# Kernel tuning notes

Hardware: AMD Instinct MI355X
Metric: run time of the kernel (lower is better)

Reference implementation:

```python
import jax, jax.numpy as jnp
import numpy as np
import math

B, S, D, H, L, V, MAXLEN = 4, 2047, 256, 8, 2, 32000, 2048
DK = D // H
DFF = 2 * D
EPS = 1e-5


def make_pe(max_len, d):
    pos = jnp.arange(max_len, dtype=jnp.float32)[:, None]
    div = jnp.exp(jnp.arange(0, d, 2, dtype=jnp.float32) * (-math.log(10000.0) / d))
    pe = jnp.zeros((max_len, d), dtype=jnp.float32)
    pe = pe.at[:, 0::2].set(jnp.sin(pos * div))
    pe = pe.at[:, 1::2].set(jnp.cos(pos * div))
    return pe[None]  # [1, max_len, d]


def setup_inputs() -> dict:
    key = jax.random.key(0)
    ks = jax.random.split(key, 16)
    s = 0.02
    T = S + 1
    return {
        "embeddings": jax.random.normal(ks[0], (B, D), jnp.float32),
        "output_tokens": jax.random.randint(ks[1], (B, S), 0, V, jnp.int64),
        "causal_mask": jnp.tril(jnp.ones((T, T), jnp.int32))[None, None],  # [1,1,T,T]
        "key_padding_mask": jnp.ones((B, 1, 1, T), jnp.int32),
        "tok_emb": jax.random.normal(ks[2], (V, D), jnp.float32) * s,
        "pe": make_pe(MAXLEN, D),
        "Wq": jax.random.normal(ks[3], (L, D, D), jnp.float32) * s,
        "Wk": jax.random.normal(ks[4], (L, D, D), jnp.float32) * s,
        "Wv": jax.random.normal(ks[5], (L, D, D), jnp.float32) * s,
        "Wo": jax.random.normal(ks[6], (L, D, D), jnp.float32) * s,
        "bo": jnp.zeros((L, D), jnp.float32),
        "ln1_g": jnp.ones((L, D), jnp.float32),
        "ln1_b": jnp.zeros((L, D), jnp.float32),
        "W1": jax.random.normal(ks[7], (L, D, DFF), jnp.float32) * s,
        "b1": jnp.zeros((L, DFF), jnp.float32),
        "W2": jax.random.normal(ks[8], (L, DFF, D), jnp.float32) * s,
        "b2": jnp.zeros((L, D), jnp.float32),
        "ln2_g": jnp.ones((L, D), jnp.float32),
        "ln2_b": jnp.zeros((L, D), jnp.float32),
    }


def layer_norm(x, g, b):
    mu = jnp.mean(x, axis=-1, keepdims=True)
    var = jnp.mean(jnp.square(x - mu), axis=-1, keepdims=True)
    return (x - mu) * jax.lax.rsqrt(var + EPS) * g + b


def attention(x, Wq, Wk, Wv, Wo, bo, causal_mask, key_padding_mask):
    b, t, d = x.shape
    q = (x @ Wq).reshape(b, t, H, DK)
    k = (x @ Wk).reshape(b, t, H, DK)
    v = (x @ Wv).reshape(b, t, H, DK)
    scores = jnp.einsum('bqhd,bkhd->bhqk', q, k) / math.sqrt(DK)  # [B,H,T,T]
    neg = jnp.float32(-jnp.inf)
    scores = jnp.where(causal_mask == 0, neg, scores)
    scores = jnp.where(key_padding_mask == 0, neg, scores)
    attn = jax.nn.softmax(scores, axis=-1)
    out = jnp.einsum('bhqk,bkhd->bqhd', attn, v).reshape(b, t, d)
    return out @ Wo + bo


def reference(embeddings, output_tokens, causal_mask, key_padding_mask,
              tok_emb, pe, Wq, Wk, Wv, Wo, bo, ln1_g, ln1_b,
              W1, b1, W2, b2, ln2_g, ln2_b):
    emb_tok = tok_emb[output_tokens]                       # [B,S,D]
    x = jnp.concatenate([embeddings[:, None, :], emb_tok], axis=1)  # [B,T,D]
    x = x + pe[:, :x.shape[1]]
    for l in range(L):
        a = attention(x, Wq[l], Wk[l], Wv[l], Wo[l], bo[l], causal_mask, key_padding_mask)
        x = layer_norm(x + a, ln1_g[l], ln1_b[l])
        ff = jax.nn.relu(x @ W1[l] + b1[l]) @ W2[l] + b2[l]
        x = layer_norm(x + ff, ln2_g[l], ln2_b[l])
    return x[:, 1:, :]  # drop the prepended embedding position
```

## Files before the change

kernel.cpp:

```cpp
#include <hip/hip_runtime.h>
#include <cstdint>
#include <cstddef>

#define B_   4
#define S_   2047
#define T_   2048
#define D_   256
#define H_   8
#define DK_  32
#define DFF_ 512
#define L_   2

typedef short          s8v  __attribute__((ext_vector_type(8)));
typedef float          f4v  __attribute__((ext_vector_type(4)));
typedef unsigned short u4v  __attribute__((ext_vector_type(4)));
typedef unsigned short u8v  __attribute__((ext_vector_type(8)));
typedef unsigned int   u2v  __attribute__((ext_vector_type(2)));
typedef unsigned int   uint32;

union U8 { u8v v; unsigned short e[8]; };

__device__ __forceinline__ float bf2f(unsigned short h) {
    unsigned int u = ((unsigned int)h) << 16;
    float f; __builtin_memcpy(&f, &u, 4); return f;
}
__device__ __forceinline__ unsigned short f2bf(float f) {
    unsigned int u; __builtin_memcpy(&u, &f, 4);
    u += 0x7fffu + ((u >> 16) & 1u);
    return (unsigned short)(u >> 16);
}
__device__ __forceinline__ uint32 pack_bf2(float lo, float hi) {
    uint32 a, b;
    __builtin_memcpy(&a, &lo, 4); __builtin_memcpy(&b, &hi, 4);
    a += 0x8000u; b += 0x8000u;
    return __builtin_amdgcn_perm(b, a, 0x07060302);
}

#define QSCALE2 0.25503485951542068f

__global__ __launch_bounds__(256) void prep_k(
    const float* __restrict__ emb, const int* __restrict__ toks,
    const float* __restrict__ tokE, const float* __restrict__ pe,
    unsigned short* __restrict__ X,
    const float* __restrict__ Wq, const float* __restrict__ Wk,
    const float* __restrict__ Wv, const float* __restrict__ Wo,
    const float* __restrict__ W1, const float* __restrict__ W2,
    unsigned short* __restrict__ WqkvT, unsigned short* __restrict__ WoT,
    unsigned short* __restrict__ W1T, unsigned short* __restrict__ W2T)
{
    __shared__ float tile[32][33];
    if (blockIdx.x < 1024) {
        int idx = blockIdx.x * 256 + threadIdx.x;
        int d8 = (idx & 31) * 8;
        int t  = (idx >> 5) & (T_ - 1);
        int b  = idx >> 16;
        const float* src = (t == 0) ? (emb + b * D_)
                                    : (tokE + (size_t)toks[b * S_ + t - 1] * D_);
        const float* p = pe + (size_t)t * D_ + d8;
        U8 o;
#pragma unroll
        for (int j = 0; j < 8; ++j) o.e[j] = f2bf(src[d8 + j] + p[j]);
        *(u8v*)(X + (size_t)(b * T_ + t) * D_ + d8) = o.v;
        return;
    }
    int idx = blockIdx.x - 1024;
    const float* src; unsigned short* dst; int R, C, tr, tc;
    if (idx < 512) {
        int w = idx >> 7, rem = idx & 127, l = rem >> 6, t = rem & 63;
        tr = t >> 3; tc = t & 7; R = 256; C = 256;
        src = (w == 0 ? Wq : w == 1 ? Wk : w == 2 ? Wv : Wo) + (size_t)l * 65536;
        dst = (w < 3) ? WqkvT + (size_t)l * 196608 + (size_t)w * 65536
                      : WoT + (size_t)l * 65536;
    } else if (idx < 768) {
        int rem = idx - 512, l = rem >> 7, t = rem & 127;
        tr = t >> 4; tc = t & 15; R = 256; C = 512;
        src = W1 + (size_t)l * 131072; dst = W1T + (size_t)l * 131072;
    } else {
        int rem = idx - 768, l = rem >> 7, t = rem & 127;
        tr = t >> 3; tc = t & 7; R = 512; C = 256;
        src = W2 + (size_t)l * 131072; dst = W2T + (size_t)l * 131072;
    }
    int x = threadIdx.x & 31, y = threadIdx.x >> 5;
    int r0 = tr * 32, c0 = tc * 32;
#pragma unroll
    for (int i = 0; i < 32; i += 8) tile[y + i][x] = src[(size_t)(r0 + y + i) * C + c0 + x];
    __syncthreads();
#pragma unroll
    for (int i = 0; i < 32; i += 8)
        dst[(size_t)(c0 + y + i) * R + r0 + x] = f2bf(tile[x][y + i]);
}

__global__ __launch_bounds__(256) void gemm64_k(
    const unsigned short* __restrict__ A, const unsigned short* __restrict__ WT,
    const float* __restrict__ bias,
    unsigned short* __restrict__ oq, unsigned short* __restrict__ ok,
    unsigned short* __restrict__ ov, unsigned short* __restrict__ out,
    int K, int Ntot, int mode)
{
    __shared__ unsigned short At[64 * 72];
    __shared__ unsigned short Wt[64 * 72];
    const int tid = threadIdx.x;
    const int wave = tid >> 6, lane = tid & 63, l15 = lane & 15, quad = lane >> 4;
    const int m0 = blockIdx.x * 64, n0g = blockIdx.y * 64;

    f4v acc[4];
#pragma unroll
    for (int i = 0; i < 4; ++i) acc[i] = (f4v){0.f, 0.f, 0.f, 0.f};

    const int arow = tid >> 2, acg = (tid & 3) * 16;
    const unsigned short* ag = A + (size_t)(m0 + arow) * K + acg;
    const unsigned short* wg = WT + (size_t)(n0g + arow) * K + acg;
    u8v a0 = *(const u8v*)ag, a1 = *(const u8v*)(ag + 8);
    u8v w0 = *(const u8v*)wg, w1 = *(const u8v*)(wg + 8);

    const int niter = K >> 6;
    for (int kk = 0; kk < niter; ++kk) {
        *(u8v*)&At[arow * 72 + acg] = a0; *(u8v*)&At[arow * 72 + acg + 8] = a1;
        *(u8v*)&Wt[arow * 72 + acg] = w0; *(u8v*)&Wt[arow * 72 + acg + 8] = w1;
        __syncthreads();
        if (kk + 1 < niter) {
            int o = (kk + 1) * 64;
            a0 = *(const u8v*)(ag + o); a1 = *(const u8v*)(ag + o + 8);
            w0 = *(const u8v*)(wg + o); w1 = *(const u8v*)(wg + o + 8);
        }
#pragma unroll
        for (int ks = 0; ks < 2; ++ks) {
            s8v aF = *(const s8v*)&At[(wave * 16 + l15) * 72 + ks * 32 + quad * 8];
#pragma unroll
            for (int nt = 0; nt < 4; ++nt) {
                s8v wF = *(const s8v*)&Wt[(nt * 16 + l15) * 72 + ks * 32 + quad * 8];
                acc[nt] = __builtin_amdgcn_mfma_f32_16x16x32_bf16(aF, wF, acc[nt], 0, 0, 0);
            }
        }
        __syncthreads();
    }

    const int b = m0 >> 11, t0 = m0 & (T_ - 1);
    if (mode == 0) {
        int sub = blockIdx.y >> 2;
        int cb  = (blockIdx.y & 3) * 64;
        if (sub < 2) {
            unsigned short* dst = sub ? ok : oq;
            float sc = sub ? 1.f : QSCALE2;
#pragma unroll
            for (int nt = 0; nt < 4; ++nt) {
                int c = cb + nt * 16 + l15, hh = c >> 5, dk = c & 31;
#pragma unroll
                for (int r = 0; r < 4; ++r) {
                    int t = t0 + wave * 16 + quad * 4 + r;
                    dst[((size_t)(b * H_ + hh) * T_ + t) * DK_ + dk] = f2bf(acc[nt][r] * sc);
                }
            }
        } else {
            unsigned short* Vb = At;
#pragma unroll
            for (int nt = 0; nt < 4; ++nt) {
                int base = (nt * 16 + l15) * 72 + wave * 16 + quad * 4;
                *(uint32*)&Vb[base]     = pack_bf2(acc[nt][0], acc[nt][1]);
                *(uint32*)&Vb[base + 2] = pack_bf2(acc[nt][2], acc[nt][3]);
            }
            __syncthreads();
            int c = tid >> 2, chunk = tid & 3;
            int cg = cb + c, hh = cg >> 5, dk = cg & 31;
            unsigned short* dst = ov + ((size_t)(b * H_ + hh) * DK_ + dk) * T_ + t0 + chunk * 16;
            u8v v0 = *(u8v*)&Vb[c * 72 + chunk * 16];
            u8v v1 = *(u8v*)&Vb[c * 72 + chunk * 16 + 8];
            *(u8v*)dst = v0; *(u8v*)(dst + 8) = v1;
        }
    } else {
#pragma unroll
        for (int nt = 0; nt < 4; ++nt) {
            int c = n0g + nt * 16 + l15;
            float bv = bias[c];
#pragma unroll
            for (int r = 0; r < 4; ++r) {
                float v = acc[nt][r] + bv;
                v = v > 0.f ? v : 0.f;
                out[(size_t)(m0 + wave * 16 + quad * 4 + r) * Ntot + c] = f2bf(v);
            }
        }
    }
}

__global__ __launch_bounds__(512) void tail32_k(
    const unsigned short* __restrict__ AO,
    const unsigned short* __restrict__ WoTl, const float* __restrict__ bo,
    const unsigned short* __restrict__ Xres,
    const float* __restrict__ g1, const float* __restrict__ be1,
    const unsigned short* __restrict__ W1Tl, const float* __restrict__ b1,
    const unsigned short* __restrict__ W2Tl, const float* __restrict__ b2,
    const float* __restrict__ g2, const float* __restrict__ be2,
    unsigned short* __restrict__ Xout, float* __restrict__ fout, int last)
{
    __shared__ unsigned short Wt[256 * 72];
    __shared__ unsigned short As[32 * 72];
    __shared__ unsigned short X1s[32 * 264];
    __shared__ unsigned short Hs[32 * 520];
    __shared__ float LNsc[256];

    const int tid = threadIdx.x;
    const int wave = tid >> 6, lane = tid & 63, l15 = lane & 15, quad = lane >> 4;
    const int wr = wave >> 2, wc = wave & 3;
    const int m0 = blockIdx.x * 32;
    const int rbase = wr * 16 + quad * 4;

    const int wrow = tid >> 1, wcol = (tid & 1) * 32;
    const int arow = tid >> 3, acol = (tid & 7) * 8;

    f4v acc[4];
    u8v w0, w1, w2, w3, a0 = {0,0,0,0,0,0,0,0};

    const unsigned short* wgo = WoTl + (size_t)wrow * 256 + wcol;
    const unsigned short* wg1 = W1Tl + (size_t)wrow * 256 + wcol;
    const unsigned short* wg1b = W1Tl + (size_t)(256 + wrow) * 256 + wcol;
    const unsigned short* wg2 = W2Tl + (size_t)wrow * 512 + wcol;
    const unsigned short* ag  = AO + (size_t)(m0 + arow) * 256 + acol;

#define LDW(p, o) { w0 = *(const u8v*)((p)+(o)); w1 = *(const u8v*)((p)+(o)+8); \
                    w2 = *(const u8v*)((p)+(o)+16); w3 = *(const u8v*)((p)+(o)+24); }
#define STW { *(u8v*)&Wt[wrow*72+wcol] = w0; *(u8v*)&Wt[wrow*72+wcol+8] = w1; \
              *(u8v*)&Wt[wrow*72+wcol+16] = w2; *(u8v*)&Wt[wrow*72+wcol+24] = w3; }

#pragma unroll
    for (int i = 0; i < 4; ++i) acc[i] = (f4v){0.f, 0.f, 0.f, 0.f};
    LDW(wgo, 0);
    if (tid < 256) a0 = *(const u8v*)ag;
    for (int kk = 0; kk < 4; ++kk) {
        STW;
        if (tid < 256) *(u8v*)&As[arow * 72 + acol] = a0;
        __syncthreads();
        if (kk < 3) {
            LDW(wgo, (kk + 1) * 64);
            if (tid < 256) a0 = *(const u8v*)(ag + (kk + 1) * 64);
        } else {
            LDW(wg1, 0);
        }
#pragma unroll
        for (int ks = 0; ks < 2; ++ks) {
            s8v aF = *(const s8v*)&As[(wr * 16 + l15) * 72 + ks * 32 + quad * 8];
#pragma unroll
            for (int nt = 0; nt < 4; ++nt) {
                s8v wF = *(const s8v*)&Wt[(wc * 64 + nt * 16 + l15) * 72 + ks * 32 + quad * 8];
                acc[nt] = __builtin_amdgcn_mfma_f32_16x16x32_bf16(aF, wF, acc[nt], 0, 0, 0);
            }
        }
        __syncthreads();
    }
    {
        float ps[4] = {0,0,0,0}, pq[4] = {0,0,0,0};
#pragma unroll
        for (int nt = 0; nt < 4; ++nt) {
            int c = wc * 64 + nt * 16 + l15;
            float bv = bo[c];
#pragma unroll
            for (int r = 0; r < 4; ++r) {
                float v = acc[nt][r] + bv + bf2f(Xres[(size_t)(m0 + rbase + r) * D_ + c]);
                acc[nt][r] = v; ps[r] += v; pq[r] += v * v;
            }
        }
#pragma unroll
        for (int r = 0; r < 4; ++r) {
            float s = ps[r], q = pq[r];
            s += __shfl_xor(s, 1); q += __shfl_xor(q, 1);
            s += __shfl_xor(s, 2); q += __shfl_xor(q, 2);
            s += __shfl_xor(s, 4); q += __shfl_xor(q, 4);
            s += __shfl_xor(s, 8); q += __shfl_xor(q, 8);
            if (l15 == 0) { LNsc[(rbase + r) * 4 + wc] = s; LNsc[128 + (rbase + r) * 4 + wc] = q; }
        }
        __syncthreads();
#pragma unroll
        for (int r = 0; r < 4; ++r) {
            int row = rbase + r;
            float s = LNsc[row * 4] + LNsc[row * 4 + 1] + LNsc[row * 4 + 2] + LNsc[row * 4 + 3];
            float q = LNsc[128 + row * 4] + LNsc[128 + row * 4 + 1] + LNsc[128 + row * 4 + 2] + LNsc[128 + row * 4 + 3];
            float m = s * (1.f / 256.f);
            float rs = rsqrtf(q * (1.f / 256.f) - m * m + 1e-5f);
#pragma unroll
            for (int nt = 0; nt < 4; ++nt) {
                int c = wc * 64 + nt * 16 + l15;
                X1s[row * 264 + c] = f2bf((acc[nt][r] - m) * rs * g1[c] + be1[c]);
            }
        }
        __syncthreads();
    }

#pragma unroll
    for (int i = 0; i < 4; ++i) acc[i] = (f4v){0.f, 0.f, 0.f, 0.f};
    for (int kk = 0; kk < 4; ++kk) {
        STW;
        __syncthreads();
        if (kk < 3) LDW(wg1, (kk + 1) * 64) else LDW(wg1b, 0);
#pragma unroll
        for (int ks = 0; ks < 2; ++ks) {
            s8v aF = *(const s8v*)&X1s[(wr * 16 + l15) * 264 + kk * 64 + ks * 32 + quad * 8];
#pragma unroll
            for (int nt = 0; nt < 4; ++nt) {
                s8v wF = *(const s8v*)&Wt[(wc * 64 + nt * 16 + l15) * 72 + ks * 32 + quad * 8];
                acc[nt] = __builtin_amdgcn_mfma_f32_16x16x32_bf16(aF, wF, acc[nt], 0, 0, 0);
            }
        }
        __syncthreads();
    }
#pragma unroll
    for (int nt = 0; nt < 4; ++nt) {
        int c = wc * 64 + nt * 16 + l15;
        float bv = b1[c];
#pragma unroll
        for (int r = 0; r < 4; ++r) {
            float v = acc[nt][r] + bv; v = v > 0.f ? v : 0.f;
            Hs[(rbase + r) * 520 + c] = f2bf(v);
        }
    }

#pragma unroll
    for (int i = 0; i < 4; ++i) acc[i] = (f4v){0.f, 0.f, 0.f, 0.f};
    for (int kk = 0; kk < 4; ++kk) {
        STW;
        __syncthreads();
        if (kk < 3) LDW(wg1b, (kk + 1) * 64) else LDW(wg2, 0);
#pragma unroll
        for (int ks = 0; ks < 2; ++ks) {
            s8v aF = *(const s8v*)&X1s[(wr * 16 + l15) * 264 + kk * 64 + ks * 32 + quad * 8];
#pragma unroll
            for (int nt = 0; nt < 4; ++nt) {
                s8v wF = *(const s8v*)&Wt[(wc * 64 + nt * 16 + l15) * 72 + ks * 32 + quad * 8];
                acc[nt] = __builtin_amdgcn_mfma_f32_16x16x32_bf16(aF, wF, acc[nt], 0, 0, 0);
            }
        }
        __syncthreads();
    }
#pragma unroll
    for (int nt = 0; nt < 4; ++nt) {
        int c = wc * 64 + nt * 16 + l15;
        float bv = b1[256 + c];
#pragma unroll
        for (int r = 0; r < 4; ++r) {
            float v = acc[nt][r] + bv; v = v > 0.f ? v : 0.f;
            Hs[(rbase + r) * 520 + 256 + c] = f2bf(v);
        }
    }

#pragma unroll
    for (int i = 0; i < 4; ++i) acc[i] = (f4v){0.f, 0.f, 0.f, 0.f};
    for (int kk = 0; kk < 8; ++kk) {
        STW;
        __syncthreads();
        if (kk < 7) LDW(wg2, (kk + 1) * 64);
#pragma unroll
        for (int ks = 0; ks < 2; ++ks) {
            s8v aF = *(const s8v*)&Hs[(wr * 16 + l15) * 520 + kk * 64 + ks * 32 + quad * 8];
#pragma unroll
            for (int nt = 0; nt < 4; ++nt) {
                s8v wF = *(const s8v*)&Wt[(wc * 64 + nt * 16 + l15) * 72 + ks * 32 + quad * 8];
                acc[nt] = __builtin_amdgcn_mfma_f32_16x16x32_bf16(aF, wF, acc[nt], 0, 0, 0);
            }
        }
        __syncthreads();
    }
    {
        float ps[4] = {0,0,0,0}, pq[4] = {0,0,0,0};
#pragma unroll
        for (int nt = 0; nt < 4; ++nt) {
            int c = wc * 64 + nt * 16 + l15;
            float bv = b2[c];
#pragma unroll
            for (int r = 0; r < 4; ++r) {
                float v = acc[nt][r] + bv + bf2f(X1s[(rbase + r) * 264 + c]);
                acc[nt][r] = v; ps[r] += v; pq[r] += v * v;
            }
        }
#pragma unroll
        for (int r = 0; r < 4; ++r) {
            float s = ps[r], q = pq[r];
            s += __shfl_xor(s, 1); q += __shfl_xor(q, 1);
            s += __shfl_xor(s, 2); q += __shfl_xor(q, 2);
            s += __shfl_xor(s, 4); q += __shfl_xor(q, 4);
            s += __shfl_xor(s, 8); q += __shfl_xor(q, 8);
            if (l15 == 0) { LNsc[(rbase + r) * 4 + wc] = s; LNsc[128 + (rbase + r) * 4 + wc] = q; }
        }
        __syncthreads();
#pragma unroll
        for (int r = 0; r < 4; ++r) {
            int row = rbase + r;
            float s = LNsc[row * 4] + LNsc[row * 4 + 1] + LNsc[row * 4 + 2] + LNsc[row * 4 + 3];
            float q = LNsc[128 + row * 4] + LNsc[128 + row * 4 + 1] + LNsc[128 + row * 4 + 2] + LNsc[128 + row * 4 + 3];
            float m = s * (1.f / 256.f);
            float rs = rsqrtf(q * (1.f / 256.f) - m * m + 1e-5f);
#pragma unroll
            for (int nt = 0; nt < 4; ++nt) {
                int c = wc * 64 + nt * 16 + l15;
                float val = (acc[nt][r] - m) * rs * g2[c] + be2[c];
                if (!last) {
                    Xout[(size_t)(m0 + row) * D_ + c] = f2bf(val);
                } else {
                    int gr = m0 + row;
                    int t = gr & (T_ - 1), bb = gr >> 11;
                    if (t) fout[((size_t)bb * S_ + t - 1) * D_ + c] = val;
                }
            }
        }
    }
#undef LDW
#undef STW
}

#define KTP 5120
#define VTP 4864
__global__ __launch_bounds__(256) void attn_k(
    const unsigned short* __restrict__ Qh, const unsigned short* __restrict__ Kh,
    const unsigned short* __restrict__ VT, unsigned short* __restrict__ AO)
{
    __shared__ unsigned short Kt[2 * KTP];
    __shared__ unsigned short Vt[2 * VTP];
    __shared__ unsigned short Ps[4][16 * 136];

    const int tid = threadIdx.x, wave = tid >> 6, lane = tid & 63;
    const int l15 = lane & 15, quad = lane >> 4;
    const int bh = blockIdx.y, b = bh >> 3, h = bh & 7;
    const size_t hoff = (size_t)bh * T_ * DK_;
    unsigned short* Pw = &Ps[wave][0];

    const int qts[2] = { (int)blockIdx.x, 31 - (int)blockIdx.x };
    const int nk0 = qts[0] / 2 + 1, nk1 = qts[1] / 2 + 1;
    const int ntot = nk0 + nk1;

    const int krow = tid >> 1, khalf = (tid & 1) * 16;
    const int vdk = tid >> 3, vc = (tid & 7) * 16;
    const unsigned short* kgp = Kh + hoff + (size_t)krow * DK_ + khalf;
    const unsigned short* vgp = VT + ((size_t)bh * DK_ + vdk) * T_ + vc;

    u8v kr0 = *(const u8v*)kgp, kr1 = *(const u8v*)(kgp + 8);
    u8v vr0 = *(const u8v*)vgp, vr1 = *(const u8v*)(vgp + 8);

    s8v qB = {0,0,0,0,0,0,0,0};
    f4v O0 = {0,0,0,0}, O1 = {0,0,0,0};
    float l_i = 0.f;
    int nkt = 0, q0w = 0;

    for (int it = 0; it < ntot; ++it) {
        const int phase = (it >= nk0);
        const int kt = phase ? it - nk0 : it;
        unsigned short* Ktb = Kt + (it & 1) * KTP;
        unsigned short* Vtb = Vt + (it & 1) * VTP;
        if (kt == 0) {
            int qt = qts[phase]; nkt = phase ? nk1 : nk0;
            q0w = qt * 64 + wave * 16;
            qB = *(const s8v*)(Qh + hoff + (size_t)(q0w + l15) * DK_ + quad * 8);
            O0 = (f4v){0,0,0,0}; O1 = (f4v){0,0,0,0};
            l_i = 0.f;
        }
        *(u8v*)&Ktb[krow * 40 + khalf]     = kr0;
        *(u8v*)&Ktb[krow * 40 + khalf + 8] = kr1;
        *(u8v*)&Vtb[vdk * 152 + vc]        = vr0;
        *(u8v*)&Vtb[vdk * 152 + vc + 8]    = vr1;
        __syncthreads();
        {
            int itn = it + 1;
            if (itn < ntot) {
                int ktn = (itn >= nk0) ? itn - nk0 : itn;
                const unsigned short* kn = kgp + (size_t)ktn * 128 * DK_;
                const unsigned short* vn = vgp + (size_t)ktn * 128;
                kr0 = *(const u8v*)kn; kr1 = *(const u8v*)(kn + 8);
                vr0 = *(const u8v*)vn; vr1 = *(const u8v*)(vn + 8);
            }
        }
        const int k0 = kt * 128;

        f4v s[8];
        f4v zero = {0,0,0,0};
#pragma unroll
        for (int nt = 0; nt < 8; ++nt) {
            s8v kA = *(const s8v*)&Ktb[(nt * 16 + l15) * 40 + quad * 8];
            s[nt] = __builtin_amdgcn_mfma_f32_16x16x32_bf16(kA, qB, zero, 0, 0, 0);
        }
        if (kt == nkt - 1) {
            int query = q0w + l15;
#pragma unroll
            for (int nt = 0; nt < 8; ++nt)
#pragma unroll
                for (int r = 0; r < 4; ++r) {
                    int key = k0 + nt * 16 + quad * 4 + r;
                    if (key > query) s[nt][r] = -1e30f;
                }
        }
        float rs = 0.f;
#pragma unroll
        for (int nt = 0; nt < 8; ++nt)
#pragma unroll
            for (int r = 0; r < 4; ++r) {
                float p = exp2f(s[nt][r]);
                s[nt][r] = p;
                rs += p;
            }
        rs += __shfl_xor(rs, 16);
        rs += __shfl_xor(rs, 32);
        l_i += rs;
#pragma unroll
        for (int nt = 0; nt < 8; ++nt) {
            u2v pw;
            pw.x = pack_bf2(s[nt][0], s[nt][1]);
            pw.y = pack_bf2(s[nt][2], s[nt][3]);
            *(u2v*)&Pw[l15 * 136 + nt * 16 + quad * 4] = pw;
        }
#pragma unroll
        for (int ks = 0; ks < 4; ++ks) {
            s8v aP = *(const s8v*)&Pw[l15 * 136 + ks * 32 + quad * 8];
            s8v v0 = *(const s8v*)&Vtb[l15 * 152 + ks * 32 + quad * 8];
            s8v v1 = *(const s8v*)&Vtb[(16 + l15) * 152 + ks * 32 + quad * 8];
            O0 = __builtin_amdgcn_mfma_f32_16x16x32_bf16(aP, v0, O0, 0, 0, 0);
            O1 = __builtin_amdgcn_mfma_f32_16x16x32_bf16(aP, v1, O1, 0, 0, 0);
        }
        if (kt == nkt - 1) {
#pragma unroll
            for (int r = 0; r < 4; ++r) {
                float linv = 1.f / __shfl(l_i, quad * 4 + r);
                int row = q0w + quad * 4 + r;
                size_t base = (size_t)(b * T_ + row) * D_ + h * DK_;
                AO[base + l15]      = f2bf(O0[r] * linv);
                AO[base + 16 + l15] = f2bf(O1[r] * linv);
            }
        }
    }
}

extern "C" void kernel_launch(void* const* d_in, const int* in_sizes, int n_in,
                              void* d_out, int out_size, void* d_ws, size_t ws_size,
                              hipStream_t stream)
{
    const float* emb  = (const float*)d_in[0];
    const int*   toks = (const int*)d_in[1];
    const float* tokE = (const float*)d_in[4];
    const float* pe   = (const float*)d_in[5];
    const float* Wq   = (const float*)d_in[6];
    const float* Wk   = (const float*)d_in[7];
    const float* Wv   = (const float*)d_in[8];
    const float* Wo   = (const float*)d_in[9];
    const float* bo   = (const float*)d_in[10];
    const float* g1   = (const float*)d_in[11];
    const float* be1  = (const float*)d_in[12];
    const float* W1   = (const float*)d_in[13];
    const float* b1   = (const float*)d_in[14];
    const float* W2   = (const float*)d_in[15];
    const float* b2   = (const float*)d_in[16];
    const float* g2   = (const float*)d_in[17];
    const float* be2  = (const float*)d_in[18];
    float* out = (float*)d_out;

    unsigned short* ws = (unsigned short*)d_ws;
    size_t off = 0;
    const size_t XSZ = (size_t)B_ * T_ * D_;
    unsigned short* Xa    = ws + off; off += XSZ;
    unsigned short* Xb    = ws + off; off += XSZ;
    unsigned short* Qh    = ws + off; off += XSZ;
    unsigned short* Kh    = ws + off; off += XSZ;
    unsigned short* VTb   = ws + off; off += XSZ;
    unsigned short* AOb   = ws + off; off += XSZ;
    unsigned short* Hb    = ws + off; off += (size_t)B_ * T_ * DFF_;
    unsigned short* WqkvT = ws + off; off += (size_t)L_ * 3 * D_ * D_;
    unsigned short* WoT   = ws + off; off += (size_t)L_ * D_ * D_;
    unsigned short* W1T   = ws + off; off += (size_t)L_ * D_ * DFF_;
    unsigned short* W2T   = ws + off; off += (size_t)L_ * DFF_ * D_;
    (void)ws_size; (void)in_sizes; (void)n_in; (void)out_size;
    (void)Xb; (void)Hb;

    prep_k<<<dim3(2048), 256, 0, stream>>>(emb, toks, tokE, pe, Xa,
                                           Wq, Wk, Wv, Wo, W1, W2,
                                           WqkvT, WoT, W1T, W2T);

    for (int l = 0; l < L_; ++l) {
        const unsigned short* wqkv = WqkvT + (size_t)l * 3 * D_ * D_;
        const unsigned short* wo   = WoT + (size_t)l * D_ * D_;
        const unsigned short* w1   = W1T + (size_t)l * D_ * DFF_;
        const unsigned short* w2   = W2T + (size_t)l * DFF_ * D_;
        const int last = (l == L_ - 1);

        gemm64_k<<<dim3(128, 12), 256, 0, stream>>>(Xa, wqkv, nullptr,
                                                    Qh, Kh, VTb, nullptr, D_, D_, 0);
        attn_k<<<dim3(16, 32), 256, 0, stream>>>(Qh, Kh, VTb, AOb);
        tail32_k<<<dim3(256), 512, 0, stream>>>(AOb, wo, bo + l * D_, Xa,
                                                g1 + l * D_, be1 + l * D_,
                                                w1, b1 + l * DFF_,
                                                w2, b2 + l * D_,
                                                g2 + l * D_, be2 + l * D_,
                                                Xa, out, last);
    }
}
```

Measured before the change: 260.0 us.

## Fuse all layer stages into one persistent cooperative kernel with grid syncs

Replaces the per-layer QKV GEMM, attention and tail kernel launches with a single cooperative kernel of 256 blocks of 512 threads. It loops over layers and separates the stages with grid-wide syncs. The goal is to remove launch overhead and inter-kernel gaps. In exchange, the work is re-partitioned onto a fixed grid: attention tiles grow from 64 to 128 query rows and lose double-buffered K/V. Each block now runs attention on 512 threads, and the grid barriers may leave stages unbalanced.

```diff
diff --git a/kernel.cpp b/kernel.cpp
--- a/kernel.cpp
+++ b/kernel.cpp
@@ -1,6 +1,9 @@
 #include <hip/hip_runtime.h>
+#include <hip/hip_cooperative_groups.h>
 #include <cstdint>
 #include <cstddef>
+
+namespace cg = cooperative_groups;
 
 #define B_   4
 #define S_   2047
@@ -13,7 +16,6 @@
 
 typedef short          s8v  __attribute__((ext_vector_type(8)));
 typedef float          f4v  __attribute__((ext_vector_type(4)));
-typedef unsigned short u4v  __attribute__((ext_vector_type(4)));
 typedef unsigned short u8v  __attribute__((ext_vector_type(8)));
 typedef unsigned int   u2v  __attribute__((ext_vector_type(2)));
 typedef unsigned int   uint32;
@@ -90,436 +92,401 @@
         dst[(size_t)(c0 + y + i) * R + r0 + x] = f2bf(tile[x][y + i]);
 }
 
-__global__ __launch_bounds__(256) void gemm64_k(
-    const unsigned short* __restrict__ A, const unsigned short* __restrict__ WT,
-    const float* __restrict__ bias,
-    unsigned short* __restrict__ oq, unsigned short* __restrict__ ok,
-    unsigned short* __restrict__ ov, unsigned short* __restrict__ out,
-    int K, int Ntot, int mode)
+struct LArgs {
+    const unsigned short *WqkvT, *WoT, *W1T, *W2T;
+    const float *bo, *g1, *be1, *b1, *b2, *g2, *be2;
+    unsigned short *Xa, *Qh, *Kh, *VT, *AO;
+    float *out;
+};
+
+__global__ __launch_bounds__(512, 2) void layers_k(LArgs A)
 {
-    __shared__ unsigned short At[64 * 72];
-    __shared__ unsigned short Wt[64 * 72];
+    __shared__ unsigned short SM[28928];
+    cg::grid_group grid = cg::this_grid();
+
     const int tid = threadIdx.x;
     const int wave = tid >> 6, lane = tid & 63, l15 = lane & 15, quad = lane >> 4;
-    const int m0 = blockIdx.x * 64, n0g = blockIdx.y * 64;
-
-    f4v acc[4];
-#pragma unroll
-    for (int i = 0; i < 4; ++i) acc[i] = (f4v){0.f, 0.f, 0.f, 0.f};
-
-    const int arow = tid >> 2, acg = (tid & 3) * 16;
-    const unsigned short* ag = A + (size_t)(m0 + arow) * K + acg;
-    const unsigned short* wg = WT + (size_t)(n0g + arow) * K + acg;
-    u8v a0 = *(const u8v*)ag, a1 = *(const u8v*)(ag + 8);
-    u8v w0 = *(const u8v*)wg, w1 = *(const u8v*)(wg + 8);
-
-    const int niter = K >> 6;
-    for (int kk = 0; kk < niter; ++kk) {
-        *(u8v*)&At[arow * 72 + acg] = a0; *(u8v*)&At[arow * 72 + acg + 8] = a1;
-        *(u8v*)&Wt[arow * 72 + acg] = w0; *(u8v*)&Wt[arow * 72 + acg + 8] = w1;
-        __syncthreads();
-        if (kk + 1 < niter) {
-            int o = (kk + 1) * 64;
-            a0 = *(const u8v*)(ag + o); a1 = *(const u8v*)(ag + o + 8);
-            w0 = *(const u8v*)(wg + o); w1 = *(const u8v*)(wg + o + 8);
+    const int bx = blockIdx.x;
+
+    for (int l = 0; l < L_; ++l) {
+        {
+            const unsigned short* WqkvTl = A.WqkvT + (size_t)l * 3 * D_ * D_;
+            const int g = tid >> 8, ltid = tid & 255;
+            const int wl = wave & 3;
+            unsigned short* At = SM + g * 9216;
+            unsigned short* Wt = At + 4608;
+            const int arow = ltid >> 2, acg = (ltid & 3) * 16;
+            for (int u = 0; u < 3; ++u) {
+                const int idx = u * 512 + bx * 2 + g;
+                const int y = idx >> 7, m0 = (idx & 127) * 64;
+                const unsigned short* ag = A.Xa + (size_t)(m0 + arow) * D_ + acg;
+                const unsigned short* wg = WqkvTl + (size_t)(y * 64 + arow) * D_ + acg;
+                u8v a0 = *(const u8v*)ag, a1 = *(const u8v*)(ag + 8);
+                u8v w0 = *(const u8v*)wg, w1 = *(const u8v*)(wg + 8);
+                f4v acc[4];
+#pragma unroll
+                for (int i = 0; i < 4; ++i) acc[i] = (f4v){0.f, 0.f, 0.f, 0.f};
+#pragma unroll
+                for (int kk = 0; kk < 4; ++kk) {
+                    *(u8v*)&At[arow * 72 + acg] = a0; *(u8v*)&At[arow * 72 + acg + 8] = a1;
+                    *(u8v*)&Wt[arow * 72 + acg] = w0; *(u8v*)&Wt[arow * 72 + acg + 8] = w1;
+                    __syncthreads();
+                    if (kk < 3) {
+                        int o = (kk + 1) * 64;
+                        a0 = *(const u8v*)(ag + o); a1 = *(const u8v*)(ag + o + 8);
+                        w0 = *(const u8v*)(wg + o); w1 = *(const u8v*)(wg + o + 8);
+                    }
+#pragma unroll
+                    for (int ks = 0; ks < 2; ++ks) {
+                        s8v aF = *(const s8v*)&At[(wl * 16 + l15) * 72 + ks * 32 + quad * 8];
+#pragma unroll
+                        for (int nt = 0; nt < 4; ++nt) {
+                            s8v wF = *(const s8v*)&Wt[(nt * 16 + l15) * 72 + ks * 32 + quad * 8];
+                            acc[nt] = __builtin_amdgcn_mfma_f32_16x16x32_bf16(aF, wF, acc[nt], 0, 0, 0);
+                        }
+                    }
+                    __syncthreads();
+                }
+                const int b = m0 >> 11, t0 = m0 & (T_ - 1);
+                const int sub = y >> 2, cb = (y & 3) * 64;
+                if (sub < 2) {
+                    unsigned short* dst = sub ? A.Kh : A.Qh;
+                    float sc = sub ? 1.f : QSCALE2;
+#pragma unroll
+                    for (int nt = 0; nt < 4; ++nt) {
+                        int c = cb + nt * 16 + l15, hh = c >> 5, dk = c & 31;
+#pragma unroll
+                        for (int r = 0; r < 4; ++r) {
+                            int t = t0 + wl * 16 + quad * 4 + r;
+                            dst[((size_t)(b * H_ + hh) * T_ + t) * DK_ + dk] = f2bf(acc[nt][r] * sc);
+                        }
+                    }
+                } else {
+                    unsigned short* Vb = At;
+#pragma unroll
+                    for (int nt = 0; nt < 4; ++nt) {
+                        int base = (nt * 16 + l15) * 72 + wl * 16 + quad * 4;
+                        *(uint32*)&Vb[base]     = pack_bf2(acc[nt][0], acc[nt][1]);
+                        *(uint32*)&Vb[base + 2] = pack_bf2(acc[nt][2], acc[nt][3]);
+                    }
+                }
+                __syncthreads();
+                if (sub == 2) {
+                    unsigned short* Vb = At;
+                    int c = ltid >> 2, chunk = ltid & 3;
+                    int cg2 = cb + c, hh = cg2 >> 5, dk = cg2 & 31;
+                    unsigned short* dst = A.VT + ((size_t)(b * H_ + hh) * DK_ + dk) * T_ + t0 + chunk * 16;
+                    u8v v0 = *(u8v*)&Vb[c * 72 + chunk * 16];
+                    u8v v1 = *(u8v*)&Vb[c * 72 + chunk * 16 + 8];
+                    *(u8v*)dst = v0; *(u8v*)(dst + 8) = v1;
+                }
+                __syncthreads();
+            }
         }
-#pragma unroll
-        for (int ks = 0; ks < 2; ++ks) {
-            s8v aF = *(const s8v*)&At[(wave * 16 + l15) * 72 + ks * 32 + quad * 8];
-#pragma unroll
-            for (int nt = 0; nt < 4; ++nt) {
-                s8v wF = *(const s8v*)&Wt[(nt * 16 + l15) * 72 + ks * 32 + quad * 8];
-                acc[nt] = __builtin_amdgcn_mfma_f32_16x16x32_bf16(aF, wF, acc[nt], 0, 0, 0);
+        grid.sync();
+
+        {
+            unsigned short* Kt = SM;
+            unsigned short* Vt = SM + 5120;
+            unsigned short* Pw = SM + 9984 + wave * 2176;
+            const int bh = bx & 31, qp = bx >> 5;
+            const int b = bh >> 3, h = bh & 7;
+            const size_t hoff = (size_t)bh * T_ * DK_;
+            const int krow = tid >> 2, kcol = (tid & 3) * 8;
+            const int vdk = tid >> 4, vc = (tid & 15) * 8;
+            const unsigned short* kgp = A.Kh + hoff + (size_t)krow * DK_ + kcol;
+            const unsigned short* vgp = A.VT + ((size_t)bh * DK_ + vdk) * T_ + vc;
+#pragma unroll
+            for (int pu = 0; pu < 2; ++pu) {
+                const int qt = pu ? 15 - qp : qp;
+                const int nkt = qt + 1;
+                const int q0w = qt * 128 + wave * 16;
+                s8v qB = *(const s8v*)(A.Qh + hoff + (size_t)(q0w + l15) * DK_ + quad * 8);
+                f4v O0 = {0,0,0,0}, O1 = {0,0,0,0};
+                float l_i = 0.f;
+                u8v kr = *(const u8v*)kgp;
+                u8v vr = *(const u8v*)vgp;
+                for (int kt = 0; kt < nkt; ++kt) {
+                    *(u8v*)&Kt[krow * 40 + kcol] = kr;
+                    *(u8v*)&Vt[vdk * 152 + vc]   = vr;
+                    __syncthreads();
+                    if (kt + 1 < nkt) {
+                        kr = *(const u8v*)(kgp + (size_t)(kt + 1) * 128 * DK_);
+                        vr = *(const u8v*)(vgp + (kt + 1) * 128);
+                    }
+                    f4v s[8];
+                    f4v zero = {0,0,0,0};
+#pragma unroll
+                    for (int nt = 0; nt < 8; ++nt) {
+                        s8v kA = *(const s8v*)&Kt[(nt * 16 + l15) * 40 + quad * 8];
+                        s[nt] = __builtin_amdgcn_mfma_f32_16x16x32_bf16(kA, qB, zero, 0, 0, 0);
+                    }
+                    if (kt == nkt - 1) {
+                        int query = q0w + l15;
+#pragma unroll
+                        for (int nt = 0; nt < 8; ++nt)
+#pragma unroll
+                            for (int r = 0; r < 4; ++r) {
+                                int key = kt * 128 + nt * 16 + quad * 4 + r;
+                                if (key > query) s[nt][r] = -1e30f;
+                            }
+                    }
+                    float rs = 0.f;
+#pragma unroll
+                    for (int nt = 0; nt < 8; ++nt)
+#pragma unroll
+                        for (int r = 0; r < 4; ++r) {
+                            float p = exp2f(s[nt][r]);
+                            s[nt][r] = p;
+                            rs += p;
+                        }
+                    rs += __shfl_xor(rs, 16);
+                    rs += __shfl_xor(rs, 32);
+                    l_i += rs;
+#pragma unroll
+                    for (int nt = 0; nt < 8; ++nt) {
+                        u2v pw;
+                        pw.x = pack_bf2(s[nt][0], s[nt][1]);
+                        pw.y = pack_bf2(s[nt][2], s[nt][3]);
+                        *(u2v*)&Pw[l15 * 136 + nt * 16 + quad * 4] = pw;
+                    }
+#pragma unroll
+                    for (int ks = 0; ks < 4; ++ks) {
+                        s8v aP = *(const s8v*)&Pw[l15 * 136 + ks * 32 + quad * 8];
+                        s8v v0 = *(const s8v*)&Vt[l15 * 152 + ks * 32 + quad * 8];
+                        s8v v1 = *(const s8v*)&Vt[(16 + l15) * 152 + ks * 32 + quad * 8];
+                        O0 = __builtin_amdgcn_mfma_f32_16x16x32_bf16(aP, v0, O0, 0, 0, 0);
+                        O1 = __builtin_amdgcn_mfma_f32_16x16x32_bf16(aP, v1, O1, 0, 0, 0);
+                    }
+                    __syncthreads();
+                }
+#pragma unroll
+                for (int r = 0; r < 4; ++r) {
+                    float linv = 1.f / __shfl(l_i, quad * 4 + r);
+                    int row = q0w + quad * 4 + r;
+                    size_t base = (size_t)(b * T_ + row) * D_ + h * DK_;
+                    A.AO[base + l15]      = f2bf(O0[r] * linv);
+                    A.AO[base + 16 + l15] = f2bf(O1[r] * linv);
+                }
             }
         }
-        __syncthreads();
-    }
-
-    const int b = m0 >> 11, t0 = m0 & (T_ - 1);
-    if (mode == 0) {
-        int sub = blockIdx.y >> 2;
-        int cb  = (blockIdx.y & 3) * 64;
-        if (sub < 2) {
-            unsigned short* dst = sub ? ok : oq;
-            float sc = sub ? 1.f : QSCALE2;
-#pragma unroll
-            for (int nt = 0; nt < 4; ++nt) {
-                int c = cb + nt * 16 + l15, hh = c >> 5, dk = c & 31;
-#pragma unroll
-                for (int r = 0; r < 4; ++r) {
-                    int t = t0 + wave * 16 + quad * 4 + r;
-                    dst[((size_t)(b * H_ + hh) * T_ + t) * DK_ + dk] = f2bf(acc[nt][r] * sc);
-                }
-            }
-        } else {
-            unsigned short* Vb = At;
-#pragma unroll
-            for (int nt = 0; nt < 4; ++nt) {
-                int base = (nt * 16 + l15) * 72 + wave * 16 + quad * 4;
-                *(uint32*)&Vb[base]     = pack_bf2(acc[nt][0], acc[nt][1]);
-                *(uint32*)&Vb[base + 2] = pack_bf2(acc[nt][2], acc[nt][3]);
-            }
-            __syncthreads();
-            int c = tid >> 2, chunk = tid & 3;
-            int cg = cb + c, hh = cg >> 5, dk = cg & 31;
-            unsigned short* dst = ov + ((size_t)(b * H_ + hh) * DK_ + dk) * T_ + t0 + chunk * 16;
-            u8v v0 = *(u8v*)&Vb[c * 72 + chunk * 16];
-            u8v v1 = *(u8v*)&Vb[c * 72 + chunk * 16 + 8];
-            *(u8v*)dst = v0; *(u8v*)(dst + 8) = v1;
-        }
-    } else {
-#pragma unroll
-        for (int nt = 0; nt < 4; ++nt) {
-            int c = n0g + nt * 16 + l15;
-            float bv = bias[c];
-#pragma unroll
-            for (int r = 0; r < 4; ++r) {
-                float v = acc[nt][r] + bv;
-                v = v > 0.f ? v : 0.f;
-                out[(size_t)(m0 + wave * 16 + quad * 4 + r) * Ntot + c] = f2bf(v);
-            }
-        }
-    }
-}
-
-__global__ __launch_bounds__(512) void tail32_k(
-    const unsigned short* __restrict__ AO,
-    const unsigned short* __restrict__ WoTl, const float* __restrict__ bo,
-    const unsigned short* __restrict__ Xres,
-    const float* __restrict__ g1, const float* __restrict__ be1,
-    const unsigned short* __restrict__ W1Tl, const float* __restrict__ b1,
-    const unsigned short* __restrict__ W2Tl, const float* __restrict__ b2,
-    const float* __restrict__ g2, const float* __restrict__ be2,
-    unsigned short* __restrict__ Xout, float* __restrict__ fout, int last)
-{
-    __shared__ unsigned short Wt[256 * 72];
-    __shared__ unsigned short As[32 * 72];
-    __shared__ unsigned short X1s[32 * 264];
-    __shared__ unsigned short Hs[32 * 520];
-    __shared__ float LNsc[256];
-
-    const int tid = threadIdx.x;
-    const int wave = tid >> 6, lane = tid & 63, l15 = lane & 15, quad = lane >> 4;
-    const int wr = wave >> 2, wc = wave & 3;
-    const int m0 = blockIdx.x * 32;
-    const int rbase = wr * 16 + quad * 4;
-
-    const int wrow = tid >> 1, wcol = (tid & 1) * 32;
-    const int arow = tid >> 3, acol = (tid & 7) * 8;
-
-    f4v acc[4];
-    u8v w0, w1, w2, w3, a0 = {0,0,0,0,0,0,0,0};
-
-    const unsigned short* wgo = WoTl + (size_t)wrow * 256 + wcol;
-    const unsigned short* wg1 = W1Tl + (size_t)wrow * 256 + wcol;
-    const unsigned short* wg1b = W1Tl + (size_t)(256 + wrow) * 256 + wcol;
-    const unsigned short* wg2 = W2Tl + (size_t)wrow * 512 + wcol;
-    const unsigned short* ag  = AO + (size_t)(m0 + arow) * 256 + acol;
-
-#define LDW(p, o) { w0 = *(const u8v*)((p)+(o)); w1 = *(const u8v*)((p)+(o)+8); \
-                    w2 = *(const u8v*)((p)+(o)+16); w3 = *(const u8v*)((p)+(o)+24); }
-#define STW { *(u8v*)&Wt[wrow*72+wcol] = w0; *(u8v*)&Wt[wrow*72+wcol+8] = w1; \
-              *(u8v*)&Wt[wrow*72+wcol+16] = w2; *(u8v*)&Wt[wrow*72+wcol+24] = w3; }
-
-#pragma unroll
-    for (int i = 0; i < 4; ++i) acc[i] = (f4v){0.f, 0.f, 0.f, 0.f};
-    LDW(wgo, 0);
-    if (tid < 256) a0 = *(const u8v*)ag;
-    for (int kk = 0; kk < 4; ++kk) {
-        STW;
-        if (tid < 256) *(u8v*)&As[arow * 72 + acol] = a0;
-        __syncthreads();
-        if (kk < 3) {
-            LDW(wgo, (kk + 1) * 64);
-            if (tid < 256) a0 = *(const u8v*)(ag + (kk + 1) * 64);
-        } else {
-            LDW(wg1, 0);
-        }
-#pragma unroll
-        for (int ks = 0; ks < 2; ++ks) {
-            s8v aF = *(const s8v*)&As[(wr * 16 + l15) * 72 + ks * 32 + quad * 8];
-#pragma unroll
-            for (int nt = 0; nt < 4; ++nt) {
-                s8v wF = *(const s8v*)&Wt[(wc * 64 + nt * 16 + l15) * 72 + ks * 32 + quad * 8];
-                acc[nt] = __builtin_amdgcn_mfma_f32_16x16x32_bf16(aF, wF, acc[nt], 0, 0, 0);
-            }
-        }
-        __syncthreads();
-    }
-    {
-        float ps[4] = {0,0,0,0}, pq[4] = {0,0,0,0};
-#pragma unroll
-        for (int nt = 0; nt < 4; ++nt) {
-            int c = wc * 64 + nt * 16 + l15;
-            float bv = bo[c];
-#pragma unroll
-            for (int r = 0; r < 4; ++r) {
-                float v = acc[nt][r] + bv + bf2f(Xres[(size_t)(m0 + rbase + r) * D_ + c]);
-                acc[nt][r] = v; ps[r] += v; pq[r] += v * v;
-            }
-        }
-#pragma unroll
-        for (int r = 0; r < 4; ++r) {
-            float s = ps[r], q = pq[r];
-            s += __shfl_xor(s, 1); q += __shfl_xor(q, 1);
-            s += __shfl_xor(s, 2); q += __shfl_xor(q, 2);
-            s += __shfl_xor(s, 4); q += __shfl_xor(q, 4);
-            s += __shfl_xor(s, 8); q += __shfl_xor(q, 8);
-            if (l15 == 0) { LNsc[(rbase + r) * 4 + wc] = s; LNsc[128 + (rbase + r) * 4 + wc] = q; }
-        }
-        __syncthreads();
-#pragma unroll
-        for (int r = 0; r < 4; ++r) {
-            int row = rbase + r;
-            float s = LNsc[row * 4] + LNsc[row * 4 + 1] + LNsc[row * 4 + 2] + LNsc[row * 4 + 3];
-            float q = LNsc[128 + row * 4] + LNsc[128 + row * 4 + 1] + LNsc[128 + row * 4 + 2] + LNsc[128 + row * 4 + 3];
-            float m = s * (1.f / 256.f);
-            float rs = rsqrtf(q * (1.f / 256.f) - m * m + 1e-5f);
+        grid.sync();
+
+        {
+            unsigned short* Wt  = SM;
+            unsigned short* As  = SM + 10240;
+            unsigned short* X1s = SM + 11520;
+            unsigned short* Hs  = SM + 19968;
+            float* LNsc = (float*)(SM + 28416);
+
+            const unsigned short* WoTl = A.WoT + (size_t)l * D_ * D_;
+            const unsigned short* W1Tl = A.W1T + (size_t)l * D_ * DFF_;
+            const unsigned short* W2Tl = A.W2T + (size_t)l * DFF_ * D_;
+            const float* pbo = A.bo + l * D_;
+            const float* pg1 = A.g1 + l * D_;  const float* pe1 = A.be1 + l * D_;
+            const float* pb1 = A.b1 + l * DFF_;
+            const float* pb2 = A.b2 + l * D_;
+            const float* pg2 = A.g2 + l * D_;  const float* pe2 = A.be2 + l * D_;
+
+            const int wr = wave >> 2, wc = wave & 3;
+            const int m0 = bx * 32;
+            const int rbase = wr * 16 + quad * 4;
+            const int wrow = tid >> 1, wcol = (tid & 1) * 16;
+            const int arow = tid >> 2, acol = (tid & 3) * 8;
+
+            const unsigned short* wgo  = WoTl + (size_t)wrow * 256 + wcol;
+            const unsigned short* wg1  = W1Tl + (size_t)wrow * 256 + wcol;
+            const unsigned short* wg1b = wg1 + 256 * 256;
+            const unsigned short* wg2  = W2Tl + (size_t)wrow * 512 + wcol;
+            const unsigned short* ag   = A.AO + (size_t)(m0 + arow) * D_ + acol;
+
+            f4v accA[4], accU[4];
+            u8v w0, w1, a0 = {0,0,0,0,0,0,0,0};
+
+#define TLDW(p, o) { w0 = *(const u8v*)((p) + (o)); w1 = *(const u8v*)((p) + (o) + 8); }
+#define TSTW { *(u8v*)&Wt[wrow * 40 + wcol] = w0; *(u8v*)&Wt[wrow * 40 + wcol + 8] = w1; }
+
+#pragma unroll
+            for (int i = 0; i < 4; ++i) accA[i] = (f4v){0.f, 0.f, 0.f, 0.f};
+            TLDW(wgo, 0);
+            if (tid < 128) a0 = *(const u8v*)ag;
+#pragma unroll
+            for (int kk = 0; kk < 8; ++kk) {
+                TSTW;
+                if (tid < 128) *(u8v*)&As[arow * 40 + acol] = a0;
+                __syncthreads();
+                if (kk < 7) { TLDW(wgo, (kk + 1) * 32); if (tid < 128) a0 = *(const u8v*)(ag + (kk + 1) * 32); }
+                else        { TLDW(wg1, 0); }
+                s8v aF = *(const s8v*)&As[(wr * 16 + l15) * 40 + quad * 8];
+#pragma unroll
+                for (int nt = 0; nt < 4; ++nt) {
+                    s8v wF = *(const s8v*)&Wt[(wc * 64 + nt * 16 + l15) * 40 + quad * 8];
+                    accA[nt] = __builtin_amdgcn_mfma_f32_16x16x32_bf16(aF, wF, accA[nt], 0, 0, 0);
+                }
+                __syncthreads();
+            }
+            {
+                float ps[4] = {0,0,0,0}, pq[4] = {0,0,0,0};
+#pragma unroll
+                for (int nt = 0; nt < 4; ++nt) {
+                    int c = wc * 64 + nt * 16 + l15;
+                    float bv = pbo[c];
+#pragma unroll
+                    for (int r = 0; r < 4; ++r) {
+                        float v = accA[nt][r] + bv + bf2f(A.Xa[(size_t)(m0 + rbase + r) * D_ + c]);
+                        accA[nt][r] = v; ps[r] += v; pq[r] += v * v;
+                    }
+                }
+#pragma unroll
+                for (int r = 0; r < 4; ++r) {
+                    float s = ps[r], q = pq[r];
+                    s += __shfl_xor(s, 1); q += __shfl_xor(q, 1);
+                    s += __shfl_xor(s, 2); q += __shfl_xor(q, 2);
+                    s += __shfl_xor(s, 4); q += __shfl_xor(q, 4);
+                    s += __shfl_xor(s, 8); q += __shfl_xor(q, 8);
+                    if (l15 == 0) { LNsc[(rbase + r) * 4 + wc] = s; LNsc[128 + (rbase + r) * 4 + wc] = q; }
+                }
+                __syncthreads();
+#pragma unroll
+                for (int r = 0; r < 4; ++r) {
+                    int row = rbase + r;
+                    float s = LNsc[row * 4] + LNsc[row * 4 + 1] + LNsc[row * 4 + 2] + LNsc[row * 4 + 3];
+                    float q = LNsc[128 + row * 4] + LNsc[128 + row * 4 + 1] + LNsc[128 + row * 4 + 2] + LNsc[128 + row * 4 + 3];
+                    float m = s * (1.f / 256.f);
+                    float rsg = rsqrtf(q * (1.f / 256.f) - m * m + 1e-5f);
+#pragma unroll
+                    for (int nt = 0; nt < 4; ++nt) {
+                        int c = wc * 64 + nt * 16 + l15;
+                        X1s[row * 264 + c] = f2bf((accA[nt][r] - m) * rsg * pg1[c] + pe1[c]);
+                    }
+                }
+                __syncthreads();
+            }
+#pragma unroll
+            for (int i = 0; i < 4; ++i) accA[i] = (f4v){0.f, 0.f, 0.f, 0.f};
+#pragma unroll
+            for (int kk = 0; kk < 8; ++kk) {
+                TSTW;
+                __syncthreads();
+                if (kk < 7) { TLDW(wg1, (kk + 1) * 32); } else { TLDW(wg2, 0); }
+                s8v aF = *(const s8v*)&X1s[(wr * 16 + l15) * 264 + kk * 32 + quad * 8];
+#pragma unroll
+                for (int nt = 0; nt < 4; ++nt) {
+                    s8v wF = *(const s8v*)&Wt[(wc * 64 + nt * 16 + l15) * 40 + quad * 8];
+                    accA[nt] = __builtin_amdgcn_mfma_f32_16x16x32_bf16(aF, wF, accA[nt], 0, 0, 0);
+                }
+                __syncthreads();
+            }
 #pragma unroll
             for (int nt = 0; nt < 4; ++nt) {
                 int c = wc * 64 + nt * 16 + l15;
-                X1s[row * 264 + c] = f2bf((acc[nt][r] - m) * rs * g1[c] + be1[c]);
-            }
-        }
-        __syncthreads();
-    }
-
-#pragma unroll
-    for (int i = 0; i < 4; ++i) acc[i] = (f4v){0.f, 0.f, 0.f, 0.f};
-    for (int kk = 0; kk < 4; ++kk) {
-        STW;
-        __syncthreads();
-        if (kk < 3) LDW(wg1, (kk + 1) * 64) else LDW(wg1b, 0);
-#pragma unroll
-        for (int ks = 0; ks < 2; ++ks) {
-            s8v aF = *(const s8v*)&X1s[(wr * 16 + l15) * 264 + kk * 64 + ks * 32 + quad * 8];
-#pragma unroll
-            for (int nt = 0; nt < 4; ++nt) {
-                s8v wF = *(const s8v*)&Wt[(wc * 64 + nt * 16 + l15) * 72 + ks * 32 + quad * 8];
-                acc[nt] = __builtin_amdgcn_mfma_f32_16x16x32_bf16(aF, wF, acc[nt], 0, 0, 0);
-            }
-        }
-        __syncthreads();
-    }
-#pragma unroll
-    for (int nt = 0; nt < 4; ++nt) {
-        int c = wc * 64 + nt * 16 + l15;
-        float bv = b1[c];
-#pragma unroll
-        for (int r = 0; r < 4; ++r) {
-            float v = acc[nt][r] + bv; v = v > 0.f ? v : 0.f;
-            Hs[(rbase + r) * 520 + c] = f2bf(v);
-        }
-    }
-
-#pragma unroll
-    for (int i = 0; i < 4; ++i) acc[i] = (f4v){0.f, 0.f, 0.f, 0.f};
-    for (int kk = 0; kk < 4; ++kk) {
-        STW;
-        __syncthreads();
-        if (kk < 3) LDW(wg1b, (kk + 1) * 64) else LDW(wg2, 0);
-#pragma unroll
-        for (int ks = 0; ks < 2; ++ks) {
-            s8v aF = *(const s8v*)&X1s[(wr * 16 + l15) * 264 + kk * 64 + ks * 32 + quad * 8];
-#pragma unroll
-            for (int nt = 0; nt < 4; ++nt) {
-                s8v wF = *(const s8v*)&Wt[(wc * 64 + nt * 16 + l15) * 72 + ks * 32 + quad * 8];
-                acc[nt] = __builtin_amdgcn_mfma_f32_16x16x32_bf16(aF, wF, acc[nt], 0, 0, 0);
-            }
-        }
-        __syncthreads();
-    }
-#pragma unroll
-    for (int nt = 0; nt < 4; ++nt) {
-        int c = wc * 64 + nt * 16 + l15;
-        float bv = b1[256 + c];
-#pragma unroll
-        for (int r = 0; r < 4; ++r) {
-            float v = acc[nt][r] + bv; v = v > 0.f ? v : 0.f;
-            Hs[(rbase + r) * 520 + 256 + c] = f2bf(v);
-        }
-    }
-
-#pragma unroll
-    for (int i = 0; i < 4; ++i) acc[i] = (f4v){0.f, 0.f, 0.f, 0.f};
-    for (int kk = 0; kk < 8; ++kk) {
-        STW;
-        __syncthreads();
-        if (kk < 7) LDW(wg2, (kk + 1) * 64);
-#pragma unroll
-        for (int ks = 0; ks < 2; ++ks) {
-            s8v aF = *(const s8v*)&Hs[(wr * 16 + l15) * 520 + kk * 64 + ks * 32 + quad * 8];
-#pragma unroll
-            for (int nt = 0; nt < 4; ++nt) {
-                s8v wF = *(const s8v*)&Wt[(wc * 64 + nt * 16 + l15) * 72 + ks * 32 + quad * 8];
-                acc[nt] = __builtin_amdgcn_mfma_f32_16x16x32_bf16(aF, wF, acc[nt], 0, 0, 0);
-            }
-        }
-        __syncthreads();
-    }
-    {
-        float ps[4] = {0,0,0,0}, pq[4] = {0,0,0,0};
-#pragma unroll
-        for (int nt = 0; nt < 4; ++nt) {
-            int c = wc * 64 + nt * 16 + l15;
-            float bv = b2[c];
-#pragma unroll
-            for (int r = 0; r < 4; ++r) {
-                float v = acc[nt][r] + bv + bf2f(X1s[(rbase + r) * 264 + c]);
-                acc[nt][r] = v; ps[r] += v; pq[r] += v * v;
-            }
-        }
-#pragma unroll
-        for (int r = 0; r < 4; ++r) {
-            float s = ps[r], q = pq[r];
-            s += __shfl_xor(s, 1); q += __shfl_xor(q, 1);
-            s += __shfl_xor(s, 2); q += __shfl_xor(q, 2);
-            s += __shfl_xor(s, 4); q += __shfl_xor(q, 4);
-            s += __shfl_xor(s, 8); q += __shfl_xor(q, 8);
-            if (l15 == 0) { LNsc[(rbase + r) * 4 + wc] = s; LNsc[128 + (rbase + r) * 4 + wc] = q; }
-        }
-        __syncthreads();
-#pragma unroll
-        for (int r = 0; r < 4; ++r) {
-            int row = rbase + r;
-            float s = LNsc[row * 4] + LNsc[row * 4 + 1] + LNsc[row * 4 + 2] + LNsc[row * 4 + 3];
-            float q = LNsc[128 + row * 4] + LNsc[128 + row * 4 + 1] + LNsc[128 + row * 4 + 2] + LNsc[128 + row * 4 + 3];
-            float m = s * (1.f / 256.f);
-            float rs = rsqrtf(q * (1.f / 256.f) - m * m + 1e-5f);
+                float bv = pb1[c];
+#pragma unroll
+                for (int r = 0; r < 4; ++r) {
+                    float v = accA[nt][r] + bv; v = v > 0.f ? v : 0.f;
+                    Hs[(rbase + r) * 264 + c] = f2bf(v);
+                }
+            }
+#pragma unroll
+            for (int i = 0; i < 4; ++i) accU[i] = (f4v){0.f, 0.f, 0.f, 0.f};
+#pragma unroll
+            for (int kk = 0; kk < 8; ++kk) {
+                TSTW;
+                __syncthreads();
+                if (kk < 7) { TLDW(wg2, (kk + 1) * 32); } else { TLDW(wg1b, 0); }
+                s8v aF = *(const s8v*)&Hs[(wr * 16 + l15) * 264 + kk * 32 + quad * 8];
+#pragma unroll
+                for (int nt = 0; nt < 4; ++nt) {
+                    s8v wF = *(const s8v*)&Wt[(wc * 64 + nt * 16 + l15) * 40 + quad * 8];
+                    accU[nt] = __builtin_amdgcn_mfma_f32_16x16x32_bf16(aF, wF, accU[nt], 0, 0, 0);
+                }
+                __syncthreads();
+            }
+#pragma unroll
+            for (int i = 0; i < 4; ++i) accA[i] = (f4v){0.f, 0.f, 0.f, 0.f};
+#pragma unroll
+            for (int kk = 0; kk < 8; ++kk) {
+                TSTW;
+                __syncthreads();
+                if (kk < 7) { TLDW(wg1b, (kk + 1) * 32); } else { TLDW(wg2, 256); }
+                s8v aF = *(const s8v*)&X1s[(wr * 16 + l15) * 264 + kk * 32 + quad * 8];
+#pragma unroll
+                for (int nt = 0; nt < 4; ++nt) {
+                    s8v wF = *(const s8v*)&Wt[(wc * 64 + nt * 16 + l15) * 40 + quad * 8];
+                    accA[nt] = __builtin_amdgcn_mfma_f32_16x16x32_bf16(aF, wF, accA[nt], 0, 0, 0);
+                }
+                __syncthreads();
+            }
 #pragma unroll
             for (int nt = 0; nt < 4; ++nt) {
                 int c = wc * 64 + nt * 16 + l15;
-                float val = (acc[nt][r] - m) * rs * g2[c] + be2[c];
-                if (!last) {
-                    Xout[(size_t)(m0 + row) * D_ + c] = f2bf(val);
-                } else {
-                    int gr = m0 + row;
-                    int t = gr & (T_ - 1), bb = gr >> 11;
-                    if (t) fout[((size_t)bb * S_ + t - 1) * D_ + c] = val;
-                }
-            }
+                float bv = pb1[256 + c];
+#pragma unroll
+                for (int r = 0; r < 4; ++r) {
+                    float v = accA[nt][r] + bv; v = v > 0.f ? v : 0.f;
+                    Hs[(rbase + r) * 264 + c] = f2bf(v);
+                }
+            }
+#pragma unroll
+            for (int kk = 0; kk < 8; ++kk) {
+                TSTW;
+                __syncthreads();
+                if (kk < 7) { TLDW(wg2, 256 + (kk + 1) * 32); }
+                s8v aF = *(const s8v*)&Hs[(wr * 16 + l15) * 264 + kk * 32 + quad * 8];
+#pragma unroll
+                for (int nt = 0; nt < 4; ++nt) {
+                    s8v wF = *(const s8v*)&Wt[(wc * 64 + nt * 16 + l15) * 40 + quad * 8];
+                    accU[nt] = __builtin_amdgcn_mfma_f32_16x16x32_bf16(aF, wF, accU[nt], 0, 0, 0);
+                }
+                __syncthreads();
+            }
+            {
+                float ps[4] = {0,0,0,0}, pq[4] = {0,0,0,0};
+#pragma unroll
+                for (int nt = 0; nt < 4; ++nt) {
+                    int c = wc * 64 + nt * 16 + l15;
+                    float bv = pb2[c];
+#pragma unroll
+                    for (int r = 0; r < 4; ++r) {
+                        float v = accU[nt][r] + bv + bf2f(X1s[(rbase + r) * 264 + c]);
+                        accU[nt][r] = v; ps[r] += v; pq[r] += v * v;
+                    }
+                }
+#pragma unroll
+                for (int r = 0; r < 4; ++r) {
+                    float s = ps[r], q = pq[r];
+                    s += __shfl_xor(s, 1); q += __shfl_xor(q, 1);
+                    s += __shfl_xor(s, 2); q += __shfl_xor(q, 2);
+                    s += __shfl_xor(s, 4); q += __shfl_xor(q, 4);
+                    s += __shfl_xor(s, 8); q += __shfl_xor(q, 8);
+                    if (l15 == 0) { LNsc[(rbase + r) * 4 + wc] = s; LNsc[128 + (rbase + r) * 4 + wc] = q; }
+                }
+                __syncthreads();
+#pragma unroll
+                for (int r = 0; r < 4; ++r) {
+                    int row = rbase + r;
+                    float s = LNsc[row * 4] + LNsc[row * 4 + 1] + LNsc[row * 4 + 2] + LNsc[row * 4 + 3];
+                    float q = LNsc[128 + row * 4] + LNsc[128 + row * 4 + 1] + LNsc[128 + row * 4 + 2] + LNsc[128 + row * 4 + 3];
+                    float m = s * (1.f / 256.f);
+                    float rsg = rsqrtf(q * (1.f / 256.f) - m * m + 1e-5f);
+#pragma unroll
+                    for (int nt = 0; nt < 4; ++nt) {
+                        int c = wc * 64 + nt * 16 + l15;
+                        float val = (accU[nt][r] - m) * rsg * pg2[c] + pe2[c];
+                        if (l == 0) {
+                            A.Xa[(size_t)(m0 + row) * D_ + c] = f2bf(val);
+                        } else {
+                            int gr = m0 + row;
+                            int t = gr & (T_ - 1), bb = gr >> 11;
+                            if (t) A.out[((size_t)bb * S_ + t - 1) * D_ + c] = val;
+                        }
+                    }
+                }
+            }
+#undef TLDW
+#undef TSTW
         }
-    }
-#undef LDW
-#undef STW
-}
-
-#define KTP 5120
-#define VTP 4864
-__global__ __launch_bounds__(256) void attn_k(
-    const unsigned short* __restrict__ Qh, const unsigned short* __restrict__ Kh,
-    const unsigned short* __restrict__ VT, unsigned short* __restrict__ AO)
-{
-    __shared__ unsigned short Kt[2 * KTP];
-    __shared__ unsigned short Vt[2 * VTP];
-    __shared__ unsigned short Ps[4][16 * 136];
-
-    const int tid = threadIdx.x, wave = tid >> 6, lane = tid & 63;
-    const int l15 = lane & 15, quad = lane >> 4;
-    const int bh = blockIdx.y, b = bh >> 3, h = bh & 7;
-    const size_t hoff = (size_t)bh * T_ * DK_;
-    unsigned short* Pw = &Ps[wave][0];
-
-    const int qts[2] = { (int)blockIdx.x, 31 - (int)blockIdx.x };
-    const int nk0 = qts[0] / 2 + 1, nk1 = qts[1] / 2 + 1;
-    const int ntot = nk0 + nk1;
-
-    const int krow = tid >> 1, khalf = (tid & 1) * 16;
-    const int vdk = tid >> 3, vc = (tid & 7) * 16;
-    const unsigned short* kgp = Kh + hoff + (size_t)krow * DK_ + khalf;
-    const unsigned short* vgp = VT + ((size_t)bh * DK_ + vdk) * T_ + vc;
-
-    u8v kr0 = *(const u8v*)kgp, kr1 = *(const u8v*)(kgp + 8);
-    u8v vr0 = *(const u8v*)vgp, vr1 = *(const u8v*)(vgp + 8);
-
-    s8v qB = {0,0,0,0,0,0,0,0};
-    f4v O0 = {0,0,0,0}, O1 = {0,0,0,0};
-    float l_i = 0.f;
-    int nkt = 0, q0w = 0;
-
-    for (int it = 0; it < ntot; ++it) {
-        const int phase = (it >= nk0);
-        const int kt = phase ? it - nk0 : it;
-        unsigned short* Ktb = Kt + (it & 1) * KTP;
-        unsigned short* Vtb = Vt + (it & 1) * VTP;
-        if (kt == 0) {
-            int qt = qts[phase]; nkt = phase ? nk1 : nk0;
-            q0w = qt * 64 + wave * 16;
-            qB = *(const s8v*)(Qh + hoff + (size_t)(q0w + l15) * DK_ + quad * 8);
-            O0 = (f4v){0,0,0,0}; O1 = (f4v){0,0,0,0};
-            l_i = 0.f;
-        }
-        *(u8v*)&Ktb[krow * 40 + khalf]     = kr0;
-        *(u8v*)&Ktb[krow * 40 + khalf + 8] = kr1;
-        *(u8v*)&Vtb[vdk * 152 + vc]        = vr0;
-        *(u8v*)&Vtb[vdk * 152 + vc + 8]    = vr1;
-        __syncthreads();
-        {
-            int itn = it + 1;
-            if (itn < ntot) {
-                int ktn = (itn >= nk0) ? itn - nk0 : itn;
-                const unsigned short* kn = kgp + (size_t)ktn * 128 * DK_;
-                const unsigned short* vn = vgp + (size_t)ktn * 128;
-                kr0 = *(const u8v*)kn; kr1 = *(const u8v*)(kn + 8);
-                vr0 = *(const u8v*)vn; vr1 = *(const u8v*)(vn + 8);
-            }
-        }
-        const int k0 = kt * 128;
-
-        f4v s[8];
-        f4v zero = {0,0,0,0};
-#pragma unroll
-        for (int nt = 0; nt < 8; ++nt) {
-            s8v kA = *(const s8v*)&Ktb[(nt * 16 + l15) * 40 + quad * 8];
-            s[nt] = __builtin_amdgcn_mfma_f32_16x16x32_bf16(kA, qB, zero, 0, 0, 0);
-        }
-        if (kt == nkt - 1) {
-            int query = q0w + l15;
-#pragma unroll
-            for (int nt = 0; nt < 8; ++nt)
-#pragma unroll
-                for (int r = 0; r < 4; ++r) {
-                    int key = k0 + nt * 16 + quad * 4 + r;
-                    if (key > query) s[nt][r] = -1e30f;
-                }
-        }
-        float rs = 0.f;
-#pragma unroll
-        for (int nt = 0; nt < 8; ++nt)
-#pragma unroll
-            for (int r = 0; r < 4; ++r) {
-                float p = exp2f(s[nt][r]);
-                s[nt][r] = p;
-                rs += p;
-            }
-        rs += __shfl_xor(rs, 16);
-        rs += __shfl_xor(rs, 32);
-        l_i += rs;
-#pragma unroll
-        for (int nt = 0; nt < 8; ++nt) {
-            u2v pw;
-            pw.x = pack_bf2(s[nt][0], s[nt][1]);
-            pw.y = pack_bf2(s[nt][2], s[nt][3]);
-            *(u2v*)&Pw[l15 * 136 + nt * 16 + quad * 4] = pw;
-        }
-#pragma unroll
-        for (int ks = 0; ks < 4; ++ks) {
-            s8v aP = *(const s8v*)&Pw[l15 * 136 + ks * 32 + quad * 8];
-            s8v v0 = *(const s8v*)&Vtb[l15 * 152 + ks * 32 + quad * 8];
-            s8v v1 = *(const s8v*)&Vtb[(16 + l15) * 152 + ks * 32 + quad * 8];
-            O0 = __builtin_amdgcn_mfma_f32_16x16x32_bf16(aP, v0, O0, 0, 0, 0);
-            O1 = __builtin_amdgcn_mfma_f32_16x16x32_bf16(aP, v1, O1, 0, 0, 0);
-        }
-        if (kt == nkt - 1) {
-#pragma unroll
-            for (int r = 0; r < 4; ++r) {
-                float linv = 1.f / __shfl(l_i, quad * 4 + r);
-                int row = q0w + quad * 4 + r;
-                size_t base = (size_t)(b * T_ + row) * D_ + h * DK_;
-                AO[base + l15]      = f2bf(O0[r] * linv);
-                AO[base + 16 + l15] = f2bf(O1[r] * linv);
-            }
-        }
+        if (l + 1 < L_) grid.sync();
     }
 }
 
@@ -567,21 +534,13 @@
                                            Wq, Wk, Wv, Wo, W1, W2,
                                            WqkvT, WoT, W1T, W2T);
 
-    for (int l = 0; l < L_; ++l) {
-        const unsigned short* wqkv = WqkvT + (size_t)l * 3 * D_ * D_;
-        const unsigned short* wo   = WoT + (size_t)l * D_ * D_;
-        const unsigned short* w1   = W1T + (size_t)l * D_ * DFF_;
-        const unsigned short* w2   = W2T + (size_t)l * DFF_ * D_;
-        const int last = (l == L_ - 1);
-
-        gemm64_k<<<dim3(128, 12), 256, 0, stream>>>(Xa, wqkv, nullptr,
-                                                    Qh, Kh, VTb, nullptr, D_, D_, 0);
-        attn_k<<<dim3(16, 32), 256, 0, stream>>>(Qh, Kh, VTb, AOb);
-        tail32_k<<<dim3(256), 512, 0, stream>>>(AOb, wo, bo + l * D_, Xa,
-                                                g1 + l * D_, be1 + l * D_,
-                                                w1, b1 + l * DFF_,
-                                                w2, b2 + l * D_,
-                                                g2 + l * D_, be2 + l * D_,
-                                                Xa, out, last);
-    }
+    LArgs la;
+    la.WqkvT = WqkvT; la.WoT = WoT; la.W1T = W1T; la.W2T = W2T;
+    la.bo = bo; la.g1 = g1; la.be1 = be1; la.b1 = b1;
+    la.b2 = b2; la.g2 = g2; la.be2 = be2;
+    la.Xa = Xa; la.Qh = Qh; la.Kh = Kh; la.VT = VTb; la.AO = AOb;
+    la.out = out;
+    void* kargs[] = { (void*)&la };
+    hipLaunchCooperativeKernel((const void*)layers_k, dim3(256), dim3(512),
+                               kargs, 0, stream);
 }
```

Measured after the change: 454.6 us. 74.8% more time.
